# Kernel tuning notes

Measured on AMD Instinct MI355X. Metric: run time of the kernel, lower is better.

Reference implementation:

```python
import jax, jax.numpy as jnp
import numpy as np

S, P, C, H, K = 16, 512, 768, 12, 6
D = C // H


def setup_inputs() -> dict:
    key = jax.random.key(0)
    k0, k1, k2 = jax.random.split(key, 3)
    x = jax.random.normal(k0, (1, S * P, C), jnp.float32)
    Wqkv = jax.random.normal(k1, (C, 3 * C), jnp.float32) * (C ** -0.5)
    bqkv = jnp.zeros((3 * C,), jnp.float32)
    Wproj = jax.random.normal(k2, (C, C), jnp.float32) * (C ** -0.5)
    bproj = jnp.zeros((C,), jnp.float32)
    # each frame i is covisible with K frames (itself + K-1 temporal neighbours)
    covis_idx = jnp.asarray((np.arange(S)[:, None] + np.arange(K)[None, :]) % S,
                            jnp.int32)  # [S, K]
    return {"x": x, "Wqkv": Wqkv, "bqkv": bqkv,
            "Wproj": Wproj, "bproj": bproj, "covis_idx": covis_idx}


def reference(x, Wqkv, bqkv, Wproj, bproj, covis_idx):
    B, N, C_ = x.shape
    S_, K_ = covis_idx.shape
    P_ = N // S_
    # qkv projection -> [3, B, H, N, D]
    qkv = (x @ Wqkv + bqkv).reshape(B, N, 3, H, D).transpose(2, 0, 3, 1, 4)
    q, k, v = qkv[0], qkv[1], qkv[2]
    kf = k.reshape(B, H, S_, P_, D)          # keys grouped by frame
    vf = v.reshape(B, H, S_, P_, D)
    qf = q.reshape(B, H, S_, P_, D).transpose(2, 0, 1, 3, 4)  # [S,B,H,P,D]
    scale = jnp.float32(D) ** -0.5

    def step(_, inp):
        q_i, idx = inp                        # q_i [B,H,P,D], idx [K]
        k_c = kf[:, :, idx].reshape(B, H, K_ * P_, D)   # gather covisible tokens
        v_c = vf[:, :, idx].reshape(B, H, K_ * P_, D)
        s = jnp.einsum('bhpd,bhnd->bhpn', q_i, k_c) * scale
        a = jax.nn.softmax(s, axis=-1)
        return None, jnp.einsum('bhpn,bhnd->bhpd', a, v_c)

    _, out = jax.lax.scan(step, None, (qf, covis_idx))  # [S,B,H,P,D]
    out = out.transpose(1, 0, 3, 2, 4).reshape(B, N, C_)  # [B, S*P, H*D]
    return out @ Wproj + bproj
```

## Files before the change

kernel.cpp:

```cpp
#include <hip/hip_runtime.h>
#include <stdint.h>

typedef __bf16 bf16;
typedef __bf16 bf16x8 __attribute__((ext_vector_type(8)));
typedef float floatx4 __attribute__((ext_vector_type(4)));

#define NTOK 8192
#define HEADSZ 524288L

__device__ __forceinline__ void gload16(const bf16* g, bf16* l) {
  __builtin_amdgcn_global_load_lds(
      (const __attribute__((address_space(1))) uint8_t*)g,
      (__attribute__((address_space(3))) uint8_t*)l, 16, 0, 0);
}

__global__ void detect_kernel(const unsigned short* __restrict__ x, int* __restrict__ flag) {
  int lane = threadIdx.x & 63;
  int cnt = 0;
#pragma unroll
  for (int i = 0; i < 4; ++i) {
    unsigned int u = x[2 * (lane * 4 + i)];
    float v = __uint_as_float(u << 16);
    if (!(fabsf(v) <= 1e4f)) cnt++;
  }
#pragma unroll
  for (int off = 1; off < 64; off <<= 1) cnt += __shfl_xor(cnt, off, 64);
  if (threadIdx.x == 0) *flag = (cnt > 32) ? 1 : 0;
}

__global__ __launch_bounds__(256) void ingest_kernel(
    const void* s0, const void* s1, const void* s2, const void* s3, const void* s4,
    bf16* d0, bf16* d1, bf16* d2, bf16* d3, bf16* d4,
    const int* __restrict__ flag) {
  const long b0 = 6291456, b1 = b0 + 1769472, b2 = b1 + 2304, b3 = b2 + 589824, b4 = b3 + 768;
  long g = ((long)blockIdx.x * 256 + threadIdx.x) * 8;
  if (g >= b4) return;
  const void* src; bf16* dst; long off;
  if (g < b0)      { src = s0; dst = d0; off = g; }
  else if (g < b1) { src = s1; dst = d1; off = g - b0; }
  else if (g < b2) { src = s2; dst = d2; off = g - b1; }
  else if (g < b3) { src = s3; dst = d3; off = g - b2; }
  else             { src = s4; dst = d4; off = g - b3; }
  if (*flag) {
    const float* s = (const float*)src + off;
#pragma unroll
    for (int e = 0; e < 8; ++e) dst[off + e] = (bf16)s[e];
  } else {
    *(uint4*)(dst + off) = *(const uint4*)((const bf16*)src + off);
  }
}

__global__ __launch_bounds__(256) void transpose_kernel(
    const bf16* __restrict__ in, bf16* __restrict__ out, int R, int Ccols) {
  __shared__ bf16 t[32][33];
  int bx = blockIdx.x * 32, by = blockIdx.y * 32;
  int tx = threadIdx.x & 31, ty = threadIdx.x >> 5;
#pragma unroll
  for (int i = ty; i < 32; i += 8) t[i][tx] = in[(long)(by + i) * Ccols + bx + tx];
  __syncthreads();
#pragma unroll
  for (int i = ty; i < 32; i += 8) out[(long)(bx + i) * R + by + tx] = t[tx][i];
}

template <int EPI>
__global__ __launch_bounds__(256, 2) void gemm_kernel(
    const bf16* __restrict__ A, const bf16* __restrict__ BT,
    const bf16* __restrict__ bias, void* __restrict__ Cout,
    int M, int N, int Kd, const int* __restrict__ flag) {
  __shared__ bf16 As[128 * 32];
  __shared__ bf16 Bs[128 * 32];
  const int tid = threadIdx.x;
  const int w = tid >> 6, lane = tid & 63;
  const int quad = lane >> 4, l15 = lane & 15;
  const int m0 = blockIdx.x * 128, n0 = blockIdx.y * 128;
  const int wm = w >> 1, wn = w & 1;
  const int srow = lane >> 2;
  const int scol = (lane & 3) * 8;

  floatx4 acc[4][4] = {};
  const bf16* ga = A + (long)(m0 + 32 * w + srow) * Kd + scol;
  const bf16* gb = BT + (long)(n0 + 32 * w + srow) * Kd + scol;
  bf16* la = As + 32 * w * 32;
  bf16* lb = Bs + 32 * w * 32;

  for (int kk = 0; kk < Kd; kk += 32) {
    __syncthreads();
    gload16(ga + kk, la);
    gload16(ga + kk + 16 * Kd, la + 16 * 32);
    gload16(gb + kk, lb);
    gload16(gb + kk + 16 * Kd, lb + 16 * 32);
    __syncthreads();
    bf16x8 fa[4], fb[4];
#pragma unroll
    for (int i = 0; i < 4; ++i)
      fa[i] = *(const bf16x8*)(As + (64 * wm + 16 * i + l15) * 32 + quad * 8);
#pragma unroll
    for (int j = 0; j < 4; ++j)
      fb[j] = *(const bf16x8*)(Bs + (64 * wn + 16 * j + l15) * 32 + quad * 8);
#pragma unroll
    for (int i = 0; i < 4; ++i)
#pragma unroll
      for (int j = 0; j < 4; ++j)
        acc[i][j] = __builtin_amdgcn_mfma_f32_16x16x32_bf16(fa[i], fb[j], acc[i][j], 0, 0, 0);
  }

  const bool outf32 = (EPI == 0) && (flag[0] != 0);
#pragma unroll
  for (int i = 0; i < 4; ++i) {
#pragma unroll
    for (int j = 0; j < 4; ++j) {
      const int col = n0 + 64 * wn + 16 * j + l15;
      const float bv = (float)bias[col];
#pragma unroll
      for (int r = 0; r < 4; ++r) {
        const int row = m0 + 64 * wm + 16 * i + quad * 4 + r;
        const float v = acc[i][j][r] + bv;
        if (EPI == 1) {
          const int which = col / 768;
          const int rem = col - which * 768;
          const int hh = rem >> 6, d = rem & 63;
          const long base = ((long)which * 12 + hh) * HEADSZ + (long)(row >> 6) * 4096;
          long off;
          if (which < 2)
            off = base + (d >> 3) * 512 + (row & 63) * 8 + (d & 7);
          else
            off = base + ((row & 63) >> 3) * 512 + d * 8 + (row & 7);
          ((bf16*)Cout)[off] = (bf16)v;
        } else {
          if (outf32) ((float*)Cout)[(long)row * N + col] = v;
          else        ((bf16*)Cout)[(long)row * N + col] = (bf16)v;
        }
      }
    }
  }
}

__global__ __launch_bounds__(256, 4) void attn_kernel(
    const bf16* __restrict__ qkv, const int* __restrict__ covis,
    bf16* __restrict__ attnout) {
  __shared__ bf16 Ks[4096];
  __shared__ bf16 Vs[4096];
  __shared__ bf16 PQ[4 * 16 * 72];
  bf16* Qs = PQ;

  const int tid = threadIdx.x;
  const int w = tid >> 6, lane = tid & 63;
  const int quad = lane >> 4, l15 = lane & 15;
  const int xcd = blockIdx.x & 7;
  const int idx = blockIdx.x >> 3;
  const int qt = idx & 7;
  const int fh = xcd * 24 + (idx >> 3);
  const int h = fh >> 4, f = fh & 15;
  const int qtb = f * 8 + qt;

  const bf16* qb = qkv + (long)(0 * 12 + h) * HEADSZ;
  const bf16* kb = qkv + (long)(1 * 12 + h) * HEADSZ;
  const bf16* vb = qkv + (long)(2 * 12 + h) * HEADSZ;

  int frames[6];
#pragma unroll
  for (int j = 0; j < 6; ++j) frames[j] = covis[f * 6 + j];

  gload16(qb + (long)qtb * 4096 + (2 * w) * 512 + lane * 8, Qs + (2 * w) * 512);
  gload16(qb + (long)qtb * 4096 + (2 * w + 1) * 512 + lane * 8, Qs + (2 * w + 1) * 512);
  __syncthreads();
  bf16x8 qa[2];
  qa[0] = *(const bf16x8*)(Qs + ((0 * 4 + quad) * 64 + 16 * w + l15) * 8);
  qa[1] = *(const bf16x8*)(Qs + ((1 * 4 + quad) * 64 + 16 * w + l15) * 8);

  bf16x8 ones;
#pragma unroll
  for (int e = 0; e < 8; ++e) ones[e] = (bf16)1.0f;

  bf16* Ps = PQ + w * 16 * 72;
  floatx4 o[4] = {};
  floatx4 osum = {};

  for (int c = 0; c < 48; ++c) {
    const int ktb = frames[c >> 3] * 8 + (c & 7);
    __syncthreads();
    gload16(kb + (long)ktb * 4096 + (2 * w) * 512 + lane * 8, Ks + (2 * w) * 512);
    gload16(kb + (long)ktb * 4096 + (2 * w + 1) * 512 + lane * 8, Ks + (2 * w + 1) * 512);
    gload16(vb + (long)ktb * 4096 + (2 * w) * 512 + lane * 8, Vs + (2 * w) * 512);
    gload16(vb + (long)ktb * 4096 + (2 * w + 1) * 512 + lane * 8, Vs + (2 * w + 1) * 512);
    __syncthreads();

#pragma unroll
    for (int nt = 0; nt < 4; ++nt) {
      bf16x8 k0 = *(const bf16x8*)(Ks + ((0 * 4 + quad) * 64 + 16 * nt + l15) * 8);
      bf16x8 k1 = *(const bf16x8*)(Ks + ((1 * 4 + quad) * 64 + 16 * nt + l15) * 8);
      floatx4 t = {};
      t = __builtin_amdgcn_mfma_f32_16x16x32_bf16(qa[0], k0, t, 0, 0, 0);
      t = __builtin_amdgcn_mfma_f32_16x16x32_bf16(qa[1], k1, t, 0, 0, 0);
#pragma unroll
      for (int r = 0; r < 4; ++r) {
        float p = __builtin_amdgcn_exp2f(t[r] * 0.18033688011112042f);
        Ps[(quad * 4 + r) * 72 + nt * 16 + l15] = (bf16)p;
      }
    }
    __syncthreads();
    bf16x8 pa0 = *(const bf16x8*)(Ps + l15 * 72 + quad * 8);
    bf16x8 pa1 = *(const bf16x8*)(Ps + l15 * 72 + 32 + quad * 8);
#pragma unroll
    for (int nt = 0; nt < 4; ++nt) {
      bf16x8 v0 = *(const bf16x8*)(Vs + ((0 * 4 + quad) * 64 + 16 * nt + l15) * 8);
      bf16x8 v1 = *(const bf16x8*)(Vs + ((1 * 4 + quad) * 64 + 16 * nt + l15) * 8);
      o[nt] = __builtin_amdgcn_mfma_f32_16x16x32_bf16(pa0, v0, o[nt], 0, 0, 0);
      o[nt] = __builtin_amdgcn_mfma_f32_16x16x32_bf16(pa1, v1, o[nt], 0, 0, 0);
    }
    osum = __builtin_amdgcn_mfma_f32_16x16x32_bf16(pa0, ones, osum, 0, 0, 0);
    osum = __builtin_amdgcn_mfma_f32_16x16x32_bf16(pa1, ones, osum, 0, 0, 0);
  }

#pragma unroll
  for (int r = 0; r < 4; ++r) {
    const float inv = 1.0f / osum[r];
    const long token = (long)qtb * 64 + 16 * w + quad * 4 + r;
#pragma unroll
    for (int nt = 0; nt < 4; ++nt)
      attnout[token * 768 + h * 64 + nt * 16 + l15] = (bf16)(o[nt][r] * inv);
  }
}

extern "C" void kernel_launch(void* const* d_in, const int* in_sizes, int n_in,
                              void* d_out, int out_size, void* d_ws, size_t ws_size,
                              hipStream_t stream) {
  const void* x     = d_in[0];
  const void* Wqkv  = d_in[1];
  const void* bqkv  = d_in[2];
  const void* Wproj = d_in[3];
  const void* bproj = d_in[4];
  const int*  covis = (const int*)d_in[5];

  char* ws = (char*)d_ws;
  size_t off = 0;
  auto alloc = [&](size_t bytes) {
    char* p = ws + off;
    off += (bytes + 255) & ~(size_t)255;
    return p;
  };
  int*  flag   = (int*)alloc(256);
  bf16* xc     = (bf16*)alloc(6291456UL * 2);
  bf16* Wqkvc  = (bf16*)alloc(1769472UL * 2);
  bf16* bqkvc  = (bf16*)alloc(2304UL * 2);
  bf16* Wprojc = (bf16*)alloc(589824UL * 2);
  bf16* bprojc = (bf16*)alloc(768UL * 2);
  bf16* WqkvT  = (bf16*)alloc(1769472UL * 2);
  bf16* WprojT = (bf16*)alloc(589824UL * 2);
  bf16* qkvws  = (bf16*)alloc(3UL * 12 * 8192 * 64 * 2);
  bf16* attnw  = (bf16*)alloc(6291456UL * 2);

  detect_kernel<<<1, 64, 0, stream>>>((const unsigned short*)x, flag);
  ingest_kernel<<<4226, 256, 0, stream>>>(x, Wqkv, bqkv, Wproj, bproj,
                                          xc, Wqkvc, bqkvc, Wprojc, bprojc, flag);
  transpose_kernel<<<dim3(72, 24), 256, 0, stream>>>(Wqkvc, WqkvT, 768, 2304);
  transpose_kernel<<<dim3(24, 24), 256, 0, stream>>>(Wprojc, WprojT, 768, 768);
  gemm_kernel<1><<<dim3(64, 18), 256, 0, stream>>>(xc, WqkvT, bqkvc, qkvws, 8192, 2304, 768, flag);
  attn_kernel<<<1536, 256, 0, stream>>>(qkvws, covis, attnw);
  gemm_kernel<0><<<dim3(64, 6), 256, 0, stream>>>(attnw, WprojT, bprojc, d_out, 8192, 768, 768, flag);
}
```

Measured before the change: 295.2 us.

## Restructure attention to split key tiles across waves with transposed S and O accumulation

The attention kernel now loads two 64-key tiles per iteration (24 iterations instead of 48). Each wave handles a quarter of the keys for all 64 queries, computing S^T with K as the A operand so the P fragments feed the PV MFMA straight from registers. This removes the LDS round-trip for P and the per-tile ones-MFMA for row sums. The exchange is 16 accumulator tiles per wave, a cross-wave LDS reduction of O and row sums at the end, and occupancy lowered to 2 blocks via larger LDS and launch bounds.

```diff
diff --git a/kernel.cpp b/kernel.cpp
--- a/kernel.cpp
+++ b/kernel.cpp
@@ -2,11 +2,28 @@
 #include <stdint.h>
 
 typedef __bf16 bf16;
+typedef __bf16 bf16x4 __attribute__((ext_vector_type(4)));
 typedef __bf16 bf16x8 __attribute__((ext_vector_type(8)));
 typedef float floatx4 __attribute__((ext_vector_type(4)));
+typedef short short4v __attribute__((ext_vector_type(4)));
 
 #define NTOK 8192
 #define HEADSZ 524288L
+
+#if defined(__has_builtin)
+#if __has_builtin(__builtin_amdgcn_mfma_f32_16x16x16bf16_1k)
+#define HAVE_MFMA16_BUILTIN 1
+#endif
+#endif
+__device__ __forceinline__ floatx4 mfma16(short4v a, short4v b, floatx4 c) {
+#ifdef HAVE_MFMA16_BUILTIN
+  return __builtin_amdgcn_mfma_f32_16x16x16bf16_1k(a, b, c, 0, 0, 0);
+#else
+  floatx4 d;
+  asm("v_mfma_f32_16x16x16_bf16 %0, %1, %2, %3" : "=v"(d) : "v"(a), "v"(b), "v"(c));
+  return d;
+#endif
+}
 
 __device__ __forceinline__ void gload16(const bf16* g, bf16* l) {
   __builtin_amdgcn_global_load_lds(
@@ -135,17 +152,17 @@
   }
 }
 
-__global__ __launch_bounds__(256, 4) void attn_kernel(
+__global__ __launch_bounds__(256, 2) void attn_kernel(
     const bf16* __restrict__ qkv, const int* __restrict__ covis,
     bf16* __restrict__ attnout) {
-  __shared__ bf16 Ks[4096];
-  __shared__ bf16 Vs[4096];
-  __shared__ bf16 PQ[4 * 16 * 72];
-  bf16* Qs = PQ;
+  __shared__ bf16 Ks[8192];
+  __shared__ bf16 Vs[8192];
 
   const int tid = threadIdx.x;
   const int w = tid >> 6, lane = tid & 63;
   const int quad = lane >> 4, l15 = lane & 15;
+  const int sb = w >> 1, hf = w & 1;
+
   const int xcd = blockIdx.x & 7;
   const int idx = blockIdx.x >> 3;
   const int qt = idx & 7;
@@ -161,64 +178,124 @@
 #pragma unroll
   for (int j = 0; j < 6; ++j) frames[j] = covis[f * 6 + j];
 
-  gload16(qb + (long)qtb * 4096 + (2 * w) * 512 + lane * 8, Qs + (2 * w) * 512);
-  gload16(qb + (long)qtb * 4096 + (2 * w + 1) * 512 + lane * 8, Qs + (2 * w + 1) * 512);
-  __syncthreads();
-  bf16x8 qa[2];
-  qa[0] = *(const bf16x8*)(Qs + ((0 * 4 + quad) * 64 + 16 * w + l15) * 8);
-  qa[1] = *(const bf16x8*)(Qs + ((1 * 4 + quad) * 64 + 16 * w + l15) * 8);
-
-  bf16x8 ones;
-#pragma unroll
-  for (int e = 0; e < 8; ++e) ones[e] = (bf16)1.0f;
-
-  bf16* Ps = PQ + w * 16 * 72;
-  floatx4 o[4] = {};
-  floatx4 osum = {};
-
-  for (int c = 0; c < 48; ++c) {
-    const int ktb = frames[c >> 3] * 8 + (c & 7);
+  bf16x8 qa[2][4];
+  {
+    const bf16* qblk = qb + (long)qtb * 4096;
+#pragma unroll
+    for (int s = 0; s < 2; ++s)
+#pragma unroll
+      for (int nt = 0; nt < 4; ++nt)
+        qa[s][nt] = *(const bf16x8*)(qblk + (4 * s + quad) * 512 + (nt * 16 + l15) * 8);
+  }
+
+  floatx4 o[16] = {};
+  float rsum[4] = {0.f, 0.f, 0.f, 0.f};
+
+  const int krow = 32 * hf + l15;
+  for (int c = 0; c < 24; ++c) {
+    const int tb0 = frames[c >> 2] * 8 + (c & 3) * 2;
     __syncthreads();
-    gload16(kb + (long)ktb * 4096 + (2 * w) * 512 + lane * 8, Ks + (2 * w) * 512);
-    gload16(kb + (long)ktb * 4096 + (2 * w + 1) * 512 + lane * 8, Ks + (2 * w + 1) * 512);
-    gload16(vb + (long)ktb * 4096 + (2 * w) * 512 + lane * 8, Vs + (2 * w) * 512);
-    gload16(vb + (long)ktb * 4096 + (2 * w + 1) * 512 + lane * 8, Vs + (2 * w + 1) * 512);
-    __syncthreads();
-
-#pragma unroll
-    for (int nt = 0; nt < 4; ++nt) {
-      bf16x8 k0 = *(const bf16x8*)(Ks + ((0 * 4 + quad) * 64 + 16 * nt + l15) * 8);
-      bf16x8 k1 = *(const bf16x8*)(Ks + ((1 * 4 + quad) * 64 + 16 * nt + l15) * 8);
-      floatx4 t = {};
-      t = __builtin_amdgcn_mfma_f32_16x16x32_bf16(qa[0], k0, t, 0, 0, 0);
-      t = __builtin_amdgcn_mfma_f32_16x16x32_bf16(qa[1], k1, t, 0, 0, 0);
-#pragma unroll
-      for (int r = 0; r < 4; ++r) {
-        float p = __builtin_amdgcn_exp2f(t[r] * 0.18033688011112042f);
-        Ps[(quad * 4 + r) * 72 + nt * 16 + l15] = (bf16)p;
-      }
+    {
+      const bf16* kg = kb + (long)tb0 * 4096 + w * 2048;
+      const bf16* vg = vb + (long)tb0 * 4096 + w * 2048;
+#pragma unroll
+      for (int i = 0; i < 4; ++i) gload16(kg + i * 512 + lane * 8, Ks + w * 2048 + i * 512);
+#pragma unroll
+      for (int i = 0; i < 4; ++i) gload16(vg + i * 512 + lane * 8, Vs + w * 2048 + i * 512);
     }
     __syncthreads();
-    bf16x8 pa0 = *(const bf16x8*)(Ps + l15 * 72 + quad * 8);
-    bf16x8 pa1 = *(const bf16x8*)(Ps + l15 * 72 + 32 + quad * 8);
-#pragma unroll
-    for (int nt = 0; nt < 4; ++nt) {
-      bf16x8 v0 = *(const bf16x8*)(Vs + ((0 * 4 + quad) * 64 + 16 * nt + l15) * 8);
-      bf16x8 v1 = *(const bf16x8*)(Vs + ((1 * 4 + quad) * 64 + 16 * nt + l15) * 8);
-      o[nt] = __builtin_amdgcn_mfma_f32_16x16x32_bf16(pa0, v0, o[nt], 0, 0, 0);
-      o[nt] = __builtin_amdgcn_mfma_f32_16x16x32_bf16(pa1, v1, o[nt], 0, 0, 0);
+
+#pragma unroll
+    for (int mt = 0; mt < 2; ++mt) {
+      floatx4 st[4] = {};
+#pragma unroll
+      for (int s = 0; s < 2; ++s) {
+        bf16x8 kf = *(const bf16x8*)(Ks + ((sb * 8 + 4 * s + quad) * 64 + krow + 16 * mt) * 8);
+#pragma unroll
+        for (int nt = 0; nt < 4; ++nt)
+          st[nt] = __builtin_amdgcn_mfma_f32_16x16x32_bf16(kf, qa[s][nt], st[nt], 0, 0, 0);
+      }
+      short4v p[4];
+#pragma unroll
+      for (int nt = 0; nt < 4; ++nt) {
+        bf16x4 pb;
+#pragma unroll
+        for (int r = 0; r < 4; ++r) {
+          float e = __builtin_amdgcn_exp2f(st[nt][r] * 0.18033688011112042f);
+          pb[r] = (bf16)e;
+          rsum[nt] += e;
+        }
+        p[nt] = __builtin_bit_cast(short4v, pb);
+      }
+#pragma unroll
+      for (int mtd = 0; mtd < 4; ++mtd) {
+        bf16x4 vf = *(const bf16x4*)(Vs + ((sb * 8 + 4 * hf + 2 * mt + (quad >> 1)) * 64 +
+                                           mtd * 16 + l15) * 8 + (quad & 1) * 4);
+        short4v va = __builtin_bit_cast(short4v, vf);
+#pragma unroll
+        for (int nt = 0; nt < 4; ++nt)
+          o[mtd * 4 + nt] = mfma16(va, p[nt], o[mtd * 4 + nt]);
+      }
     }
-    osum = __builtin_amdgcn_mfma_f32_16x16x32_bf16(pa0, ones, osum, 0, 0, 0);
-    osum = __builtin_amdgcn_mfma_f32_16x16x32_bf16(pa1, ones, osum, 0, 0, 0);
-  }
-
-#pragma unroll
-  for (int r = 0; r < 4; ++r) {
-    const float inv = 1.0f / osum[r];
-    const long token = (long)qtb * 64 + 16 * w + quad * 4 + r;
-#pragma unroll
-    for (int nt = 0; nt < 4; ++nt)
-      attnout[token * 768 + h * 64 + nt * 16 + l15] = (bf16)(o[nt][r] * inv);
+  }
+
+  __syncthreads();
+  float* sc = (float*)Ks;
+#pragma unroll
+  for (int nt = 0; nt < 4; ++nt) {
+    rsum[nt] += __shfl_xor(rsum[nt], 16, 64);
+    rsum[nt] += __shfl_xor(rsum[nt], 32, 64);
+    sc[(w * 4 + nt) * 64 + lane] = rsum[nt];
+  }
+  __syncthreads();
+  float inv[4];
+#pragma unroll
+  for (int nt = 0; nt < 4; ++nt) {
+    float tot = sc[nt * 64 + lane] + sc[(4 + nt) * 64 + lane] +
+                sc[(8 + nt) * 64 + lane] + sc[(12 + nt) * 64 + lane];
+    inv[nt] = 1.0f / tot;
+  }
+  __syncthreads();
+
+  float* buf0 = (float*)Ks;
+  float* buf1 = (float*)Vs;
+  if (w == 2) {
+#pragma unroll
+    for (int t = 0; t < 16; ++t) *(floatx4*)(buf0 + (t * 64 + lane) * 4) = o[t];
+  } else if (w == 3) {
+#pragma unroll
+    for (int t = 0; t < 16; ++t) *(floatx4*)(buf1 + (t * 64 + lane) * 4) = o[t];
+  }
+  __syncthreads();
+  if (w == 0) {
+#pragma unroll
+    for (int t = 0; t < 16; ++t) o[t] += *(const floatx4*)(buf0 + (t * 64 + lane) * 4);
+  } else if (w == 1) {
+#pragma unroll
+    for (int t = 0; t < 16; ++t) o[t] += *(const floatx4*)(buf1 + (t * 64 + lane) * 4);
+  }
+  __syncthreads();
+  if (w == 1) {
+#pragma unroll
+    for (int t = 0; t < 16; ++t) *(floatx4*)(buf0 + (t * 64 + lane) * 4) = o[t];
+  }
+  __syncthreads();
+  if (w == 0) {
+    bf16* ob = (bf16*)Vs;
+#pragma unroll
+    for (int mtd = 0; mtd < 4; ++mtd)
+#pragma unroll
+      for (int nt = 0; nt < 4; ++nt) {
+        floatx4 t = o[mtd * 4 + nt] + *(const floatx4*)(buf0 + ((mtd * 4 + nt) * 64 + lane) * 4);
+        bf16x4 bv;
+#pragma unroll
+        for (int r = 0; r < 4; ++r) bv[r] = (bf16)(t[r] * inv[nt]);
+        *(bf16x4*)(ob + (nt * 16 + l15) * 64 + mtd * 16 + quad * 4) = bv;
+      }
+    bf16* dst = attnout + ((long)qtb * 64 + lane) * 768 + h * 64;
+#pragma unroll
+    for (int i = 0; i < 8; ++i)
+      *(bf16x8*)(dst + i * 8) = *(const bf16x8*)(ob + lane * 64 + i * 8);
   }
 }
 
```

New measurement: 283.4 us. -4.0%, faster.
